# Optimization experiments

Measured on AMD Instinct MI355X. Metric: run time of the kernel, lower is better.

The kernel has to match this reference:

```python
import jax, jax.numpy as jnp
import numpy as np

B, S, H, V, C = 32, 512, 256, 50000, 5
NUM_LAYERS, WINDOW = 2, 2


def setup_inputs() -> dict:
    key = jax.random.key(0)
    ks = jax.random.split(key, 24)
    std = 0.1  # matches nn.init.normal_(p, 0, 0.1)
    n = lambda k, shp: jax.random.normal(k, shp, dtype=jnp.float32) * std
    u = lambda k, shp: -0.05 + jax.random.uniform(k, shp, dtype=jnp.float32) * 0.1
    return {
        "input_sentences": jax.random.randint(ks[0], (B, S), 0, V),
        "sentences_length": jax.random.randint(ks[1], (B,), 1, S),
        "hh0": u(ks[2], (B, S, H)),
        "cs0": u(ks[3], (B, S, H)),
        "embed": n(ks[4], (V, H)),
        # stacked word-gate weights, gate order: i, l, r, f, s, output, u
        "W_lr": n(ks[5], (7, H, 2 * H)),
        "W_c": n(ks[6], (7, H, H)),
        "W_x": n(ks[7], (7, H, H)),
        "W_g": n(ks[8], (7, H, H)),
        "gate_bias": n(ks[9], (7, H)),
        # sentence-state gates
        "W_fg_g": n(ks[10], (H, H)),
        "W_fg_h": n(ks[11], (H, H)),
        "W_fgi_g": n(ks[12], (H, H)),
        "W_fgi_h": n(ks[13], (H, H)),
        "W_og_g": n(ks[14], (H, H)),
        "W_og_h": n(ks[15], (H, H)),
        "b_fg": n(ks[16], (H,)),
        "b_fgi": n(ks[17], (H,)),
        # output head
        "W1": n(ks[18], (H, 2 * H)),
        "b1": n(ks[19], (H,)),
        "Wout": n(ks[20], (C, H)),
        "bout": n(ks[21], (C,)),
    }


def _before_sum(x, window):
    # sum of right-shifted (zero-padded at front) copies, shifts 1..window
    out = jnp.zeros_like(x)
    for s in range(1, window + 1):
        out = out + jnp.pad(x[:, :-s], ((0, 0), (s, 0), (0, 0)))
    return out


def _after_sum(x, window):
    out = jnp.zeros_like(x)
    for s in range(1, window + 1):
        out = out + jnp.pad(x[:, s:], ((0, 0), (0, s), (0, 0)))
    return out


def _slstm_step(hh, cs, sv, scs, wv, W_lr, W_c, W_x, W_g, gate_bias,
                W_fg_g, W_fg_h, W_fgi_g, W_fgi_h, W_og_g, W_og_h, b_fg, b_fgi):
    avg_hh = hh.mean(axis=1)                                   # [B,H]
    f_hat_g = jax.nn.sigmoid(sv @ W_fg_g.T + avg_hh @ W_fg_h.T + b_fg)
    # NOTE: original code (faithfully) uses output_gate_bias here, not output_gate_g_bias
    og_g = jax.nn.sigmoid(sv @ W_og_g.T + avg_hh @ W_og_h.T + gate_bias[5])
    f_hat_g_i = jax.nn.sigmoid((sv @ W_fgi_g.T)[:, None] + hh @ W_fgi_h.T + b_fgi)
    scores = jax.nn.softmax(f_hat_g_i, axis=2)                 # over hidden dim
    new_scs = jax.nn.softmax(f_hat_g, axis=1) * scs + (scores * cs).sum(axis=1)
    new_sv = og_g * jnp.tanh(new_scs)

    hb = _before_sum(hh, WINDOW)
    ha = _after_sum(hh, WINDOW)
    cb = _before_sum(cs, WINDOW)
    ca = _after_sum(cs, WINDOW)
    ba = jnp.concatenate([hb, ha], axis=-1)                    # [B,S,2H]

    # all 7 gate pre-activations at once: [B,S,7,H]
    pre = (jnp.einsum('bsk,ghk->bsgh', ba, W_lr)
           + jnp.einsum('bsk,ghk->bsgh', hh, W_c)
           + jnp.einsum('bsk,ghk->bsgh', wv, W_x)
           + (jnp.einsum('bk,ghk->bgh', new_sv, W_g) + gate_bias)[:, None])

    g5 = jax.nn.sigmoid(pre[..., :5, :])                       # i,l,r,f,s
    b_, s_ = g5.shape[:2]
    # joint softmax over the concatenated 5*H gate vector (as in torch cat+softmax)
    g5 = jax.nn.softmax(g5.reshape(b_, s_, -1), axis=-1).reshape(b_, s_, 5, -1)
    i_t, l_t, r_t, f_t, s_t = (g5[..., k, :] for k in range(5))
    og = jax.nn.sigmoid(pre[..., 5, :])
    u_g = jnp.tanh(pre[..., 6, :])

    new_cs = l_t * cb + f_t * cs + r_t * ca + s_t * scs[:, None] + i_t * u_g
    new_hh = og * jnp.tanh(new_cs)
    return new_hh, new_cs, new_sv, new_scs


def reference(input_sentences, sentences_length, hh0, cs0, embed,
              W_lr, W_c, W_x, W_g, gate_bias,
              W_fg_g, W_fg_h, W_fgi_g, W_fgi_h, W_og_g, W_og_h, b_fg, b_fgi,
              W1, b1, Wout, bout):
    wv = embed[input_sentences]                                # [B,S,H]
    hh, cs = hh0, cs0
    sv, scs = hh0.mean(axis=1), cs0.mean(axis=1)
    for _ in range(NUM_LAYERS):
        hh, cs, sv, scs = _slstm_step(hh, cs, sv, scs, wv,
                                      W_lr, W_c, W_x, W_g, gate_bias,
                                      W_fg_g, W_fg_h, W_fgi_g, W_fgi_h,
                                      W_og_g, W_og_h, b_fg, b_fgi)
    avg_hh = hh.mean(axis=1)
    conc = jnp.concatenate([avg_hh, sv], axis=1) @ W1.T + b1
    fc = conc @ Wout.T + bout
    return jax.nn.log_softmax(fc, axis=1), sv
```

## Files before the change

kernel.cpp:

```cpp
#include <hip/hip_runtime.h>
#include <stdint.h>
#include <math.h>

#define B_   32
#define S_   512
#define H_   256
#define M_   (B_*S_)
#define KBIG 1024
#define NB   1792
#define NB2  2048
#define C_   5

typedef __bf16 bf16;
typedef __bf16 bf16x4 __attribute__((ext_vector_type(4)));
typedef __bf16 bf16x8 __attribute__((ext_vector_type(8)));
typedef float  floatx4 __attribute__((ext_vector_type(4)));

__device__ __forceinline__ float sigm(float x){ return 1.f/(1.f+expf(-x)); }

__device__ __forceinline__ void gl16(const bf16* g, bf16* l){
    __builtin_amdgcn_global_load_lds(
        (const __attribute__((address_space(1))) unsigned int*)g,
        (__attribute__((address_space(3))) unsigned int*)l, 16, 0, 0);
}

__global__ void wcomb_k(const float* __restrict__ Wlr, const float* __restrict__ Wc,
                        const float* __restrict__ Wx, const float* __restrict__ Wfgi,
                        bf16* __restrict__ WT){
    int n = blockIdx.x;
    int k4 = threadIdx.x * 4;
    float4 v;
    if (n < NB){
        int g = n >> 8, h = n & 255;
        const float* src;
        if (k4 < 512)      src = Wlr + ((size_t)(g*256 + h))*512 + k4;
        else if (k4 < 768) src = Wc  + ((size_t)(g*256 + h))*256 + (k4 - 512);
        else               src = Wx  + ((size_t)(g*256 + h))*256 + (k4 - 768);
        v = *(const float4*)src;
    } else {
        int h = n - NB;
        if (k4 >= 512 && k4 < 768) v = *(const float4*)(Wfgi + (size_t)h*H_ + (k4 - 512));
        else { v.x=0.f; v.y=0.f; v.z=0.f; v.w=0.f; }
    }
    bf16 o[4] = {(bf16)v.x,(bf16)v.y,(bf16)v.z,(bf16)v.w};
    *(uint2*)&WT[(size_t)n*KBIG + k4] = *(uint2*)o;
}

__global__ void gather_k(const int* __restrict__ idx, const float* __restrict__ embed,
                         bf16* __restrict__ wv){
    int i4 = (blockIdx.x*256 + threadIdx.x)*4;
    int m = i4 >> 8, h = i4 & 255;
    float4 v = *(const float4*)(embed + (size_t)idx[m]*H_ + h);
    bf16 o[4] = {(bf16)v.x,(bf16)v.y,(bf16)v.z,(bf16)v.w};
    *(uint2*)(wv + (size_t)m*H_ + h) = *(uint2*)o;
}

__global__ void mean1_k(const float* __restrict__ x, float* __restrict__ part){
    int b = blockIdx.x, c = blockIdx.y, h = threadIdx.x;
    const float* p = x + ((size_t)b*S_ + c*32)*H_ + h;
    float s = 0.f;
    #pragma unroll 8
    for (int t=0;t<32;t++) s += p[(size_t)t*H_];
    part[((size_t)b*16 + c)*H_ + h] = s;
}
__global__ void mean2_k(const float* __restrict__ part, float* __restrict__ out){
    int b = blockIdx.x, h = threadIdx.x;
    float s = 0.f;
    #pragma unroll
    for (int c=0;c<16;c++) s += part[((size_t)b*16 + c)*H_ + h];
    out[b*H_ + h] = s * (1.f/512.f);
}

__global__ void buildx_k(const float* __restrict__ hh, const bf16* __restrict__ wv,
                         bf16* __restrict__ X){
    int m = blockIdx.x, tid = threadIdx.x;
    int seg = tid >> 6, li = tid & 63;
    int s = m & (S_-1);
    int h0 = li*4;
    size_t base = (size_t)m*H_ + h0;
    bf16* xr = X + (size_t)m*KBIG + seg*H_ + h0;
    const float4 z = {0.f,0.f,0.f,0.f};
    if (seg == 3){
        *(uint2*)xr = *(const uint2*)&wv[base];
        return;
    }
    float4 v;
    if (seg == 0){
        float4 a = (s>=1) ? *(const float4*)&hh[base - H_]   : z;
        float4 b = (s>=2) ? *(const float4*)&hh[base - 2*H_] : z;
        v.x=a.x+b.x; v.y=a.y+b.y; v.z=a.z+b.z; v.w=a.w+b.w;
    } else if (seg == 1){
        float4 a = (s<=S_-2) ? *(const float4*)&hh[base + H_]   : z;
        float4 b = (s<=S_-3) ? *(const float4*)&hh[base + 2*H_] : z;
        v.x=a.x+b.x; v.y=a.y+b.y; v.z=a.z+b.z; v.w=a.w+b.w;
    } else {
        v = *(const float4*)&hh[base];
    }
    bf16 o[4] = {(bf16)v.x,(bf16)v.y,(bf16)v.z,(bf16)v.w};
    *(uint2*)xr = *(uint2*)o;
}

__global__ void mv5_k(const float* __restrict__ sv, const float* __restrict__ avg,
    const float* __restrict__ Wfg_g, const float* __restrict__ Wfg_h,
    const float* __restrict__ Wog_g, const float* __restrict__ Wog_h,
    const float* __restrict__ Wfgi_g, float* __restrict__ res){
    int j = blockIdx.x, b = blockIdx.y, h = threadIdx.x;
    const float* vec = (j==1 || j==3) ? avg + b*H_ : sv + b*H_;
    const float* W   = (j==0)?Wfg_g:(j==1)?Wfg_h:(j==2)?Wog_g:(j==3)?Wog_h:Wfgi_g;
    __shared__ float v[H_];
    v[h] = vec[h]; __syncthreads();
    const float* w = W + (size_t)h*H_;
    float d = 0.f;
    for (int k=0;k<H_;k++) d += v[k]*w[k];
    res[((size_t)b*5 + j)*H_ + h] = d;
}
__global__ void comb_k(const float* __restrict__ res, const float* __restrict__ b_fg,
                       const float* __restrict__ gbias, const float* __restrict__ b_fgi,
                       float* __restrict__ fhg, float* __restrict__ ogg,
                       float* __restrict__ svg){
    int b = blockIdx.x, h = threadIdx.x;
    const float* r = res + (size_t)b*5*H_;
    fhg[b*H_+h] = sigm(r[h] + r[H_+h] + b_fg[h]);
    ogg[b*H_+h] = sigm(r[2*H_+h] + r[3*H_+h] + gbias[5*H_+h]);
    svg[b*H_+h] = r[4*H_+h] + b_fgi[h];
}

__device__ __forceinline__ void mmq(floatx4 (&acc)[8][4], bf16x8 (&af)[4][2], bf16x8 (&bfr)[2][2],
                                    int MH, int NH){
    #pragma unroll
    for (int mi2=0;mi2<4;mi2++)
        #pragma unroll
        for (int ni2=0;ni2<2;ni2++)
            #pragma unroll
            for (int kk=0;kk<2;kk++)
                acc[MH*4+mi2][NH*2+ni2] = __builtin_amdgcn_mfma_f32_16x16x32_bf16(
                    af[mi2][kk], bfr[ni2][kk], acc[MH*4+mi2][NH*2+ni2], 0, 0, 0);
}

__global__ __launch_bounds__(512, 2)
void mgemm256_k(const bf16* __restrict__ A, const bf16* __restrict__ BT,
                bf16* __restrict__ C, int Kdim, int lda, int ldb, int ldc, int nbx){
    __shared__ alignas(16) bf16 lsA[2][256*64];
    __shared__ alignas(16) bf16 lsB[2][256*64];
    const int tid  = threadIdx.x;
    const int lane = tid & 63;
    const int wave = tid >> 6;
    const int wm = wave >> 2;
    const int wn = wave & 3;
    const int lrow = lane & 15, quad = lane >> 4;

    const int cpx = gridDim.x >> 3;
    const int w   = (blockIdx.x & 7)*cpx + (blockIdx.x >> 3);
    const int mb  = w / nbx, nb = w - mb*nbx;
    const int m0 = mb * 256, n0 = nb * 256;

    const int srow = tid >> 3;
    const int scol = ((tid & 7) ^ (srow & 7)) * 8;
    const bf16* Ab = A  + (size_t)(m0 + srow)*lda + scol;
    const bf16* Bb = BT + (size_t)(n0 + srow)*ldb + scol;
    const int NT = Kdim >> 6;

    floatx4 zero = {0.f,0.f,0.f,0.f};
    floatx4 acc[8][4];
    #pragma unroll
    for (int i=0;i<8;i++)
        #pragma unroll
        for (int j=0;j<4;j++) acc[i][j] = zero;
    bf16x8 af[4][2], bfrA[2][2], bfrB[2][2];

#define SA_(bu,r,kt) gl16(Ab + (size_t)(r)*64*lda + (size_t)(kt)*64, &lsA[bu][(r)*4096 + tid*8])
#define SB_(bu,r,kt) gl16(Bb + (size_t)(r)*64*ldb + (size_t)(kt)*64, &lsB[bu][(r)*4096 + tid*8])
#define RA_(bu,MH,mi2,kk) (*(const bf16x8*)&lsA[bu][(wm*128 + (MH)*64 + (mi2)*16 + lrow)*64 + ((((kk)*4+quad) ^ (lrow&7))*8)])
#define RB_(bu,NH,ni2,kk) (*(const bf16x8*)&lsB[bu][(wn*64  + (NH)*32 + (ni2)*16 + lrow)*64 + ((((kk)*4+quad) ^ (lrow&7))*8)])

    SB_(0,0,0); SB_(0,1,0); SB_(0,2,0); SB_(0,3,0);
    SA_(0,0,0); SA_(0,2,0); SA_(0,1,0); SA_(0,3,0);
    asm volatile("s_waitcnt vmcnt(2)" ::: "memory");
    __builtin_amdgcn_s_barrier();

    for (int kt = 0; kt < NT; ++kt){
        const int cur = kt & 1, nxt = cur ^ 1;
        const bool st = (kt + 1 < NT);
        const int k1 = kt + 1;

        #pragma unroll
        for (int mi2=0;mi2<4;mi2++){ af[mi2][0] = RA_(cur,0,mi2,0); af[mi2][1] = RA_(cur,0,mi2,1); }
        #pragma unroll
        for (int ni2=0;ni2<2;ni2++){ bfrA[ni2][0] = RB_(cur,0,ni2,0); bfrA[ni2][1] = RB_(cur,0,ni2,1); }
        if (st){ SB_(nxt,0,k1); SB_(nxt,1,k1); }
        __builtin_amdgcn_s_barrier();
        __builtin_amdgcn_s_setprio(1);
        mmq(acc, af, bfrA, 0, 0);
        __builtin_amdgcn_s_setprio(0);
        __builtin_amdgcn_s_barrier();

        #pragma unroll
        for (int ni2=0;ni2<2;ni2++){ bfrB[ni2][0] = RB_(cur,1,ni2,0); bfrB[ni2][1] = RB_(cur,1,ni2,1); }
        if (st){ SB_(nxt,2,k1); SB_(nxt,3,k1); }
        __builtin_amdgcn_s_barrier();
        __builtin_amdgcn_s_setprio(1);
        mmq(acc, af, bfrB, 0, 1);
        __builtin_amdgcn_s_setprio(0);
        if (st) asm volatile("s_waitcnt vmcnt(4)" ::: "memory");
        else    asm volatile("s_waitcnt vmcnt(0)" ::: "memory");
        __builtin_amdgcn_s_barrier();

        #pragma unroll
        for (int mi2=0;mi2<4;mi2++){ af[mi2][0] = RA_(cur,1,mi2,0); af[mi2][1] = RA_(cur,1,mi2,1); }
        if (st){ SA_(nxt,0,k1); SA_(nxt,2,k1); }
        __builtin_amdgcn_s_barrier();
        __builtin_amdgcn_s_setprio(1);
        mmq(acc, af, bfrB, 1, 1);
        __builtin_amdgcn_s_setprio(0);
        __builtin_amdgcn_s_barrier();

        if (st){ SA_(nxt,1,k1); SA_(nxt,3,k1); }
        __builtin_amdgcn_s_barrier();
        __builtin_amdgcn_s_setprio(1);
        mmq(acc, af, bfrA, 1, 0);
        __builtin_amdgcn_s_setprio(0);
        if (st) asm volatile("s_waitcnt vmcnt(2)" ::: "memory");
        __builtin_amdgcn_s_barrier();
    }
#undef SA_
#undef SB_
#undef RA_
#undef RB_

    #pragma unroll
    for (int mi=0;mi<8;mi++)
        #pragma unroll
        for (int ni=0;ni<4;ni++){
            int row = m0 + wm*128 + mi*16 + quad*4;
            int col = n0 + wn*64  + ni*16 + lrow;
            #pragma unroll
            for (int r=0;r<4;r++)
                C[(size_t)(row+r)*ldc + col] = (bf16)acc[mi][ni][r];
        }
}

__global__ void scorep_k(const bf16* __restrict__ fgih, const float* __restrict__ svg,
                         const float* __restrict__ cs, float* __restrict__ part, int ldf){
    int chunk = blockIdx.x, b = blockIdx.y;
    int tid = threadIdx.x, wave = tid >> 6, lane = tid & 63;
    __shared__ float acc4[4][256];
    float sw[4], acc[4] = {0.f,0.f,0.f,0.f};
    #pragma unroll
    for (int j=0;j<4;j++) sw[j] = svg[b*H_ + lane + 64*j];
    for (int t=wave; t<16; t+=4){
        int m = b*S_ + chunk*16 + t;
        const bf16* fr = fgih + (size_t)m*ldf;
        float e[4], loc = 0.f;
        #pragma unroll
        for (int j=0;j<4;j++){ e[j] = expf(sigm(sw[j] + (float)fr[lane+64*j])); loc += e[j]; }
        #pragma unroll
        for (int off=32; off; off>>=1) loc += __shfl_xor(loc, off, 64);
        float inv = 1.f/loc;
        const float* cr = cs + (size_t)m*H_;
        #pragma unroll
        for (int j=0;j<4;j++) acc[j] += e[j]*inv*cr[lane+64*j];
    }
    #pragma unroll
    for (int j=0;j<4;j++) acc4[wave][lane+64*j] = acc[j];
    __syncthreads();
    part[((size_t)b*32 + chunk)*H_ + tid] =
        acc4[0][tid] + acc4[1][tid] + acc4[2][tid] + acc4[3][tid];
}

__global__ void newscs_k(const float* __restrict__ part, const float* __restrict__ fhg,
                         const float* __restrict__ ogg, const float* __restrict__ scs_in,
                         float* __restrict__ scs_out, float* __restrict__ sv_out){
    int b = blockIdx.x, h = threadIdx.x;
    __shared__ float r[256];
    float dot = 0.f;
    #pragma unroll 8
    for (int c=0;c<32;c++) dot += part[((size_t)b*32+c)*H_ + h];
    float e = expf(fhg[b*H_+h]);
    r[h] = e; __syncthreads();
    for (int off=128; off; off>>=1){ if (h<off) r[h] += r[h+off]; __syncthreads(); }
    float ns = (e / r[0]) * scs_in[b*H_+h] + dot;
    scs_out[b*H_+h] = ns;
    sv_out[b*H_+h]  = ogg[b*H_+h] * tanhf(ns);
}

__global__ void gterm_k(const float* __restrict__ svn, const float* __restrict__ Wg,
                        const float* __restrict__ gbias, float* __restrict__ gt){
    int g = blockIdx.x, b = blockIdx.y, h = threadIdx.x;
    __shared__ float s[H_];
    s[h] = svn[b*H_+h]; __syncthreads();
    const float* w = Wg + ((size_t)g*H_ + h)*H_;
    float d = 0.f;
    for (int k=0;k<H_;k++) d += s[k]*w[k];
    gt[(size_t)b*NB + g*H_ + h] = d + gbias[g*H_+h];
}

__global__ void gates_k(const bf16* __restrict__ pre, const float* __restrict__ gt,
                        const float* __restrict__ cs_in, const float* __restrict__ scs_in,
                        float* __restrict__ hh_out, float* __restrict__ cs_out, int ldp){
    int tid = threadIdx.x, wave = tid >> 6, lane = tid & 63;
    int m = blockIdx.x*4 + wave;
    int b = m >> 9, s = m & (S_-1);
    const bf16* row = pre + (size_t)m*ldp;
    int h0 = lane*4;
    float pv[7][4];
    #pragma unroll
    for (int g=0; g<7; ++g){
        bf16x4 t = *(const bf16x4*)&row[g*H_ + h0];
        float4 gq = *(const float4*)&gt[(size_t)b*NB + g*H_ + h0];
        pv[g][0] = (float)t[0] + gq.x;
        pv[g][1] = (float)t[1] + gq.y;
        pv[g][2] = (float)t[2] + gq.z;
        pv[g][3] = (float)t[3] + gq.w;
    }
    float ex[5][4], og[4], u[4];
    float loc = 0.f;
    #pragma unroll
    for (int g=0; g<5; ++g)
        #pragma unroll
        for (int j=0;j<4;j++){ float e = expf(sigm(pv[g][j])); ex[g][j] = e; loc += e; }
    #pragma unroll
    for (int j=0;j<4;j++){ og[j] = sigm(pv[5][j]); u[j] = tanhf(pv[6][j]); }
    #pragma unroll
    for (int off=32; off; off>>=1) loc += __shfl_xor(loc, off, 64);
    float inv = 1.f / loc;

    size_t i0 = (size_t)m*H_ + h0;
    const float4 z = {0.f,0.f,0.f,0.f};
    float4 c0  = *(const float4*)&cs_in[i0];
    float4 cm1 = (s>=1)    ? *(const float4*)&cs_in[i0 - H_]   : z;
    float4 cm2 = (s>=2)    ? *(const float4*)&cs_in[i0 - 2*H_] : z;
    float4 cp1 = (s<=S_-2) ? *(const float4*)&cs_in[i0 + H_]   : z;
    float4 cp2 = (s<=S_-3) ? *(const float4*)&cs_in[i0 + 2*H_] : z;
    float4 sc  = *(const float4*)&scs_in[(size_t)b*H_ + h0];
    float4 nc4, nh4;
    #pragma unroll
    for (int j=0;j<4;j++){
        float cb = ((const float*)&cm1)[j] + ((const float*)&cm2)[j];
        float ca = ((const float*)&cp1)[j] + ((const float*)&cp2)[j];
        float nc = ex[1][j]*inv*cb + ex[3][j]*inv*((const float*)&c0)[j] + ex[2][j]*inv*ca
                 + ex[4][j]*inv*((const float*)&sc)[j] + ex[0][j]*inv*u[j];
        ((float*)&nc4)[j] = nc;
        ((float*)&nh4)[j] = og[j] * tanhf(nc);
    }
    *(float4*)&cs_out[i0] = nc4;
    *(float4*)&hh_out[i0] = nh4;
}

__global__ void head_k(const float* __restrict__ avgh, const float* __restrict__ sv,
                       const float* __restrict__ W1, const float* __restrict__ b1,
                       const float* __restrict__ Wout, const float* __restrict__ bout,
                       float* __restrict__ out){
    int b = blockIdx.x, t = threadIdx.x;
    __shared__ float conc[H_];
    __shared__ float fc[8];
    const float* wr = W1 + (size_t)t*512;
    float d = b1[t];
    for (int k=0;k<H_;k++) d += avgh[b*H_+k]*wr[k];
    for (int k=0;k<H_;k++) d += sv[b*H_+k]*wr[256+k];
    conc[t] = d;
    __syncthreads();
    if (t < C_){
        const float* wo = Wout + (size_t)t*H_;
        float s = bout[t];
        for (int i=0;i<H_;i++) s += conc[i]*wo[i];
        fc[t] = s;
    }
    __syncthreads();
    if (t == 0){
        float mx = fc[0];
        for (int c=1;c<C_;c++) mx = fmaxf(mx, fc[c]);
        float se = 0.f;
        for (int c=0;c<C_;c++) se += expf(fc[c]-mx);
        float lse = mx + logf(se);
        for (int c=0;c<C_;c++) out[b*C_+c] = fc[c]-lse;
    }
    out[B_*C_ + b*H_ + t] = sv[b*H_+t];
}

extern "C" void kernel_launch(void* const* d_in, const int* in_sizes, int n_in,
                              void* d_out, int out_size, void* d_ws, size_t ws_size,
                              hipStream_t stream){
    const int*   idx    = (const int*)d_in[0];
    const float* hh0    = (const float*)d_in[2];
    const float* cs0    = (const float*)d_in[3];
    const float* embed  = (const float*)d_in[4];
    const float* Wlr    = (const float*)d_in[5];
    const float* Wc     = (const float*)d_in[6];
    const float* Wx     = (const float*)d_in[7];
    const float* Wg     = (const float*)d_in[8];
    const float* gbias  = (const float*)d_in[9];
    const float* Wfg_g  = (const float*)d_in[10];
    const float* Wfg_h  = (const float*)d_in[11];
    const float* Wfgi_g = (const float*)d_in[12];
    const float* Wfgi_h = (const float*)d_in[13];
    const float* Wog_g  = (const float*)d_in[14];
    const float* Wog_h  = (const float*)d_in[15];
    const float* b_fg   = (const float*)d_in[16];
    const float* b_fgi  = (const float*)d_in[17];
    const float* W1     = (const float*)d_in[18];
    const float* b1     = (const float*)d_in[19];
    const float* Wout   = (const float*)d_in[20];
    const float* bout   = (const float*)d_in[21];

    uint8_t* p = (uint8_t*)d_ws;
    auto alloc = [&](size_t bytes)->void*{ void* r=(void*)p; p += (bytes + 255) & ~(size_t)255; return r; };
    bf16*  WT    = (bf16*)alloc((size_t)NB2*KBIG*2);
    bf16*  X     = (bf16*)alloc((size_t)M_*KBIG*2);
    bf16*  wv    = (bf16*)alloc((size_t)M_*H_*2);
    bf16*  pre   = (bf16*)alloc((size_t)M_*NB2*2);
    float* hhA = (float*)alloc((size_t)M_*H_*4);
    float* csA = (float*)alloc((size_t)M_*H_*4);
    float* hhB = (float*)alloc((size_t)M_*H_*4);
    float* csB = (float*)alloc((size_t)M_*H_*4);
    float* mpart= (float*)alloc((size_t)B_*16*H_*4);
    float* part = (float*)alloc((size_t)B_*32*H_*4);
    float* res5 = (float*)alloc((size_t)B_*5*H_*4);
    float* avgh = (float*)alloc(B_*H_*4);
    float* fhg  = (float*)alloc(B_*H_*4);
    float* ogg  = (float*)alloc(B_*H_*4);
    float* svg  = (float*)alloc(B_*H_*4);
    float* svP0 = (float*)alloc(B_*H_*4);
    float* svP1 = (float*)alloc(B_*H_*4);
    float* scP0 = (float*)alloc(B_*H_*4);
    float* scP1 = (float*)alloc(B_*H_*4);
    float* gt   = (float*)alloc((size_t)B_*NB*4);

    wcomb_k <<<NB2,         256, 0, stream>>>(Wlr, Wc, Wx, Wfgi_h, WT);
    gather_k<<<(M_*H_)/1024,256, 0, stream>>>(idx, embed, wv);
    mean1_k <<<dim3(B_,16), 256, 0, stream>>>(hh0, mpart);
    mean2_k <<<B_,          256, 0, stream>>>(mpart, svP0);
    mean1_k <<<dim3(B_,16), 256, 0, stream>>>(cs0, mpart);
    mean2_k <<<B_,          256, 0, stream>>>(mpart, scP0);

    const float *hin = hh0, *cin = cs0;
    float *hout = hhA, *cout = csA;
    float *svin = svP0, *scin = scP0, *svout = svP1, *scout = scP1;

    for (int l=0; l<2; ++l){
        const float* avgp;
        if (l == 0){
            avgp = svin;
        } else {
            mean1_k<<<dim3(B_,16), 256, 0, stream>>>(hin, mpart);
            mean2_k<<<B_,          256, 0, stream>>>(mpart, avgh);
            avgp = avgh;
        }
        mv5_k   <<<dim3(5,B_), 256, 0, stream>>>(svin, avgp, Wfg_g, Wfg_h, Wog_g,
                                                 Wog_h, Wfgi_g, res5);
        comb_k  <<<B_, 256, 0, stream>>>(res5, b_fg, gbias, b_fgi, fhg, ogg, svg);
        buildx_k<<<M_, 256, 0, stream>>>(hin, wv, X);
        mgemm256_k<<<512, 512, 0, stream>>>(X, WT, pre, KBIG, KBIG, KBIG, NB2, 8);
        scorep_k<<<dim3(32,B_), 256, 0, stream>>>(pre + NB, svg, cin, part, NB2);
        newscs_k<<<B_, 256, 0, stream>>>(part, fhg, ogg, scin, scout, svout);
        gterm_k <<<dim3(7,B_), 256, 0, stream>>>(svout, Wg, gbias, gt);
        gates_k <<<M_/4, 256, 0, stream>>>(pre, gt, cin, scin, hout, cout, NB2);
        hin = hout; cin = cout;
        hout = (l==0) ? hhB : hhA;
        cout = (l==0) ? csB : csA;
        float* q;
        q = svin; svin = svout; svout = q;
        q = scin; scin = scout; scout = q;
    }
    mean1_k<<<dim3(B_,16), 256, 0, stream>>>(hin, mpart);
    mean2_k<<<B_,          256, 0, stream>>>(mpart, avgh);
    head_k <<<B_, 256, 0, stream>>>(avgh, svin, W1, b1, Wout, bout, (float*)d_out);
}
```

Baseline: 516.5 us.

## Simplify GEMM pipeline to one prefetch per tile and fuse gate matvecs

The main GEMM loop drops its interleaved quarter-tile prefetch, which needed many barriers. It now issues all next-tile global-to-LDS loads at the top of each iteration, waits for the previous tile, runs all four MFMA quadrants, and uses a single barrier per k-step. Separately, the five sentence-gate matvecs and their combine step are fused into one kernel per batch row, which removes a launch and the intermediate buffer. The GEMM change cuts synchronisation but may lose the finer overlap of loads with compute. The fused matvec launches only 32 blocks, so it has less parallelism.

```diff
diff --git a/kernel.cpp b/kernel.cpp
--- a/kernel.cpp
+++ b/kernel.cpp
@@ -100,29 +100,31 @@
     *(uint2*)xr = *(uint2*)o;
 }
 
-__global__ void mv5_k(const float* __restrict__ sv, const float* __restrict__ avg,
+__global__ void mv5c_k(const float* __restrict__ sv, const float* __restrict__ avg,
     const float* __restrict__ Wfg_g, const float* __restrict__ Wfg_h,
     const float* __restrict__ Wog_g, const float* __restrict__ Wog_h,
-    const float* __restrict__ Wfgi_g, float* __restrict__ res){
-    int j = blockIdx.x, b = blockIdx.y, h = threadIdx.x;
-    const float* vec = (j==1 || j==3) ? avg + b*H_ : sv + b*H_;
-    const float* W   = (j==0)?Wfg_g:(j==1)?Wfg_h:(j==2)?Wog_g:(j==3)?Wog_h:Wfgi_g;
-    __shared__ float v[H_];
-    v[h] = vec[h]; __syncthreads();
-    const float* w = W + (size_t)h*H_;
-    float d = 0.f;
-    for (int k=0;k<H_;k++) d += v[k]*w[k];
-    res[((size_t)b*5 + j)*H_ + h] = d;
-}
-__global__ void comb_k(const float* __restrict__ res, const float* __restrict__ b_fg,
-                       const float* __restrict__ gbias, const float* __restrict__ b_fgi,
-                       float* __restrict__ fhg, float* __restrict__ ogg,
-                       float* __restrict__ svg){
+    const float* __restrict__ Wfgi_g,
+    const float* __restrict__ b_fg, const float* __restrict__ gbias,
+    const float* __restrict__ b_fgi,
+    float* __restrict__ fhg, float* __restrict__ ogg, float* __restrict__ svg){
     int b = blockIdx.x, h = threadIdx.x;
-    const float* r = res + (size_t)b*5*H_;
-    fhg[b*H_+h] = sigm(r[h] + r[H_+h] + b_fg[h]);
-    ogg[b*H_+h] = sigm(r[2*H_+h] + r[3*H_+h] + gbias[5*H_+h]);
-    svg[b*H_+h] = r[4*H_+h] + b_fgi[h];
+    __shared__ float vs[H_], va[H_];
+    vs[h] = sv[b*H_+h]; va[h] = avg[b*H_+h];
+    __syncthreads();
+    const float* w0 = Wfg_g  + (size_t)h*H_;
+    const float* w1 = Wfg_h  + (size_t)h*H_;
+    const float* w2 = Wog_g  + (size_t)h*H_;
+    const float* w3 = Wog_h  + (size_t)h*H_;
+    const float* w4 = Wfgi_g + (size_t)h*H_;
+    float d0=0.f,d1=0.f,d2=0.f,d3=0.f,d4=0.f;
+    #pragma unroll 4
+    for (int k=0;k<H_;k++){
+        float s = vs[k], a = va[k];
+        d0 += s*w0[k]; d1 += a*w1[k]; d2 += s*w2[k]; d3 += a*w3[k]; d4 += s*w4[k];
+    }
+    fhg[b*H_+h] = sigm(d0 + d1 + b_fg[h]);
+    ogg[b*H_+h] = sigm(d2 + d3 + gbias[5*H_+h]);
+    svg[b*H_+h] = d4 + b_fgi[h];
 }
 
 __device__ __forceinline__ void mmq(floatx4 (&acc)[8][4], bf16x8 (&af)[4][2], bf16x8 (&bfr)[2][2],
@@ -174,8 +176,8 @@
 #define RB_(bu,NH,ni2,kk) (*(const bf16x8*)&lsB[bu][(wn*64  + (NH)*32 + (ni2)*16 + lrow)*64 + ((((kk)*4+quad) ^ (lrow&7))*8)])
 
     SB_(0,0,0); SB_(0,1,0); SB_(0,2,0); SB_(0,3,0);
-    SA_(0,0,0); SA_(0,2,0); SA_(0,1,0); SA_(0,3,0);
-    asm volatile("s_waitcnt vmcnt(2)" ::: "memory");
+    SA_(0,0,0); SA_(0,1,0); SA_(0,2,0); SA_(0,3,0);
+    asm volatile("s_waitcnt vmcnt(0)" ::: "memory");
     __builtin_amdgcn_s_barrier();
 
     for (int kt = 0; kt < NT; ++kt){
@@ -183,43 +185,36 @@
         const bool st = (kt + 1 < NT);
         const int k1 = kt + 1;
 
+        if (st){
+            SB_(nxt,0,k1); SB_(nxt,1,k1); SB_(nxt,2,k1); SB_(nxt,3,k1);
+            SA_(nxt,0,k1); SA_(nxt,1,k1); SA_(nxt,2,k1); SA_(nxt,3,k1);
+            asm volatile("s_waitcnt vmcnt(8)" ::: "memory");
+        } else {
+            asm volatile("s_waitcnt vmcnt(0)" ::: "memory");
+        }
+
         #pragma unroll
         for (int mi2=0;mi2<4;mi2++){ af[mi2][0] = RA_(cur,0,mi2,0); af[mi2][1] = RA_(cur,0,mi2,1); }
         #pragma unroll
         for (int ni2=0;ni2<2;ni2++){ bfrA[ni2][0] = RB_(cur,0,ni2,0); bfrA[ni2][1] = RB_(cur,0,ni2,1); }
-        if (st){ SB_(nxt,0,k1); SB_(nxt,1,k1); }
-        __builtin_amdgcn_s_barrier();
         __builtin_amdgcn_s_setprio(1);
         mmq(acc, af, bfrA, 0, 0);
         __builtin_amdgcn_s_setprio(0);
-        __builtin_amdgcn_s_barrier();
 
         #pragma unroll
         for (int ni2=0;ni2<2;ni2++){ bfrB[ni2][0] = RB_(cur,1,ni2,0); bfrB[ni2][1] = RB_(cur,1,ni2,1); }
-        if (st){ SB_(nxt,2,k1); SB_(nxt,3,k1); }
-        __builtin_amdgcn_s_barrier();
         __builtin_amdgcn_s_setprio(1);
         mmq(acc, af, bfrB, 0, 1);
         __builtin_amdgcn_s_setprio(0);
-        if (st) asm volatile("s_waitcnt vmcnt(4)" ::: "memory");
-        else    asm volatile("s_waitcnt vmcnt(0)" ::: "memory");
-        __builtin_amdgcn_s_barrier();
 
         #pragma unroll
         for (int mi2=0;mi2<4;mi2++){ af[mi2][0] = RA_(cur,1,mi2,0); af[mi2][1] = RA_(cur,1,mi2,1); }
-        if (st){ SA_(nxt,0,k1); SA_(nxt,2,k1); }
-        __builtin_amdgcn_s_barrier();
         __builtin_amdgcn_s_setprio(1);
         mmq(acc, af, bfrB, 1, 1);
-        __builtin_amdgcn_s_setprio(0);
-        __builtin_amdgcn_s_barrier();
-
-        if (st){ SA_(nxt,1,k1); SA_(nxt,3,k1); }
-        __builtin_amdgcn_s_barrier();
-        __builtin_amdgcn_s_setprio(1);
         mmq(acc, af, bfrA, 1, 0);
         __builtin_amdgcn_s_setprio(0);
-        if (st) asm volatile("s_waitcnt vmcnt(2)" ::: "memory");
+
+        asm volatile("s_waitcnt lgkmcnt(0)" ::: "memory");
         __builtin_amdgcn_s_barrier();
     }
 #undef SA_
@@ -414,7 +409,6 @@
     float* csB = (float*)alloc((size_t)M_*H_*4);
     float* mpart= (float*)alloc((size_t)B_*16*H_*4);
     float* part = (float*)alloc((size_t)B_*32*H_*4);
-    float* res5 = (float*)alloc((size_t)B_*5*H_*4);
     float* avgh = (float*)alloc(B_*H_*4);
     float* fhg  = (float*)alloc(B_*H_*4);
     float* ogg  = (float*)alloc(B_*H_*4);
@@ -445,9 +439,8 @@
             mean2_k<<<B_,          256, 0, stream>>>(mpart, avgh);
             avgp = avgh;
         }
-        mv5_k   <<<dim3(5,B_), 256, 0, stream>>>(svin, avgp, Wfg_g, Wfg_h, Wog_g,
-                                                 Wog_h, Wfgi_g, res5);
-        comb_k  <<<B_, 256, 0, stream>>>(res5, b_fg, gbias, b_fgi, fhg, ogg, svg);
+        mv5c_k  <<<B_, 256, 0, stream>>>(svin, avgp, Wfg_g, Wfg_h, Wog_g, Wog_h,
+                                         Wfgi_g, b_fg, gbias, b_fgi, fhg, ogg, svg);
         buildx_k<<<M_, 256, 0, stream>>>(hin, wv, X);
         mgemm256_k<<<512, 512, 0, stream>>>(X, WT, pre, KBIG, KBIG, KBIG, NB2, 8);
         scorep_k<<<dim3(32,B_), 256, 0, stream>>>(pre + NB, svg, cin, part, NB2);
```

Result: slower. 582.2 us (+12.7%).

## Replace 256x256 ping-pong GEMM with simpler 128x128 tile, K=32 kernel

Applied to the files above, without the earlier changes.

Swaps the 256x256-tile, 8-wave GEMM with its interleaved multi-barrier schedule for a 128x128-tile, 4-wave kernel that steps through K 32 at a time with plain double buffering, and launches 2048 blocks instead of 512. The aim is higher occupancy and shorter dependency chains in the per-layer projection GEMM. Each loaded byte is reused less, so global/L2 traffic rises, and there are more barriers per unit of work.

```diff
diff --git a/kernel.cpp b/kernel.cpp
--- a/kernel.cpp
+++ b/kernel.cpp
@@ -125,101 +125,66 @@
     svg[b*H_+h] = r[4*H_+h] + b_fgi[h];
 }
 
-__device__ __forceinline__ void mmq(floatx4 (&acc)[8][4], bf16x8 (&af)[4][2], bf16x8 (&bfr)[2][2],
-                                    int MH, int NH){
-    #pragma unroll
-    for (int mi2=0;mi2<4;mi2++)
-        #pragma unroll
-        for (int ni2=0;ni2<2;ni2++)
-            #pragma unroll
-            for (int kk=0;kk<2;kk++)
-                acc[MH*4+mi2][NH*2+ni2] = __builtin_amdgcn_mfma_f32_16x16x32_bf16(
-                    af[mi2][kk], bfr[ni2][kk], acc[MH*4+mi2][NH*2+ni2], 0, 0, 0);
-}
-
-__global__ __launch_bounds__(512, 2)
-void mgemm256_k(const bf16* __restrict__ A, const bf16* __restrict__ BT,
+__global__ __launch_bounds__(256, 4)
+void mgemm128_k(const bf16* __restrict__ A, const bf16* __restrict__ BT,
                 bf16* __restrict__ C, int Kdim, int lda, int ldb, int ldc, int nbx){
-    __shared__ alignas(16) bf16 lsA[2][256*64];
-    __shared__ alignas(16) bf16 lsB[2][256*64];
+    __shared__ alignas(16) bf16 lsA[2][128*32];
+    __shared__ alignas(16) bf16 lsB[2][128*32];
     const int tid  = threadIdx.x;
     const int lane = tid & 63;
     const int wave = tid >> 6;
-    const int wm = wave >> 2;
-    const int wn = wave & 3;
+    const int wmr = (wave & 1) * 64;
+    const int wnr = (wave >> 1) * 64;
     const int lrow = lane & 15, quad = lane >> 4;
 
     const int cpx = gridDim.x >> 3;
     const int w   = (blockIdx.x & 7)*cpx + (blockIdx.x >> 3);
     const int mb  = w / nbx, nb = w - mb*nbx;
-    const int m0 = mb * 256, n0 = nb * 256;
-
-    const int srow = tid >> 3;
-    const int scol = ((tid & 7) ^ (srow & 7)) * 8;
-    const bf16* Ab = A  + (size_t)(m0 + srow)*lda + scol;
-    const bf16* Bb = BT + (size_t)(n0 + srow)*ldb + scol;
-    const int NT = Kdim >> 6;
+    const int m0 = mb * 128, n0 = nb * 128;
+
+    const int srow  = tid >> 2;
+    const int sslot = (tid & 3) ^ ((srow >> 1) & 3);
+    const bf16* Ab = A  + (size_t)(m0 + srow)*lda + sslot*8;
+    const bf16* Bb = BT + (size_t)(n0 + srow)*ldb + sslot*8;
+    const int NT = Kdim >> 5;
 
     floatx4 zero = {0.f,0.f,0.f,0.f};
-    floatx4 acc[8][4];
-    #pragma unroll
-    for (int i=0;i<8;i++)
+    floatx4 acc[4][4];
+    #pragma unroll
+    for (int i=0;i<4;i++)
         #pragma unroll
         for (int j=0;j<4;j++) acc[i][j] = zero;
-    bf16x8 af[4][2], bfrA[2][2], bfrB[2][2];
-
-#define SA_(bu,r,kt) gl16(Ab + (size_t)(r)*64*lda + (size_t)(kt)*64, &lsA[bu][(r)*4096 + tid*8])
-#define SB_(bu,r,kt) gl16(Bb + (size_t)(r)*64*ldb + (size_t)(kt)*64, &lsB[bu][(r)*4096 + tid*8])
-#define RA_(bu,MH,mi2,kk) (*(const bf16x8*)&lsA[bu][(wm*128 + (MH)*64 + (mi2)*16 + lrow)*64 + ((((kk)*4+quad) ^ (lrow&7))*8)])
-#define RB_(bu,NH,ni2,kk) (*(const bf16x8*)&lsB[bu][(wn*64  + (NH)*32 + (ni2)*16 + lrow)*64 + ((((kk)*4+quad) ^ (lrow&7))*8)])
-
-    SB_(0,0,0); SB_(0,1,0); SB_(0,2,0); SB_(0,3,0);
-    SA_(0,0,0); SA_(0,2,0); SA_(0,1,0); SA_(0,3,0);
-    asm volatile("s_waitcnt vmcnt(2)" ::: "memory");
-    __builtin_amdgcn_s_barrier();
+    bf16x8 af[4], bfr[4];
+
+#define SA_(bu,r,kt) gl16(Ab + (size_t)(r)*64*lda + (size_t)(kt)*32, &lsA[bu][(r)*2048 + tid*8])
+#define SB_(bu,r,kt) gl16(Bb + (size_t)(r)*64*ldb + (size_t)(kt)*32, &lsB[bu][(r)*2048 + tid*8])
+#define RA_(bu,mi) (*(const bf16x8*)&lsA[bu][(wmr + (mi)*16 + lrow)*32 + ((quad ^ ((lrow>>1)&3))*8)])
+#define RB_(bu,ni) (*(const bf16x8*)&lsB[bu][(wnr + (ni)*16 + lrow)*32 + ((quad ^ ((lrow>>1)&3))*8)])
+
+    SA_(0,0,0); SA_(0,1,0); SB_(0,0,0); SB_(0,1,0);
 
     for (int kt = 0; kt < NT; ++kt){
         const int cur = kt & 1, nxt = cur ^ 1;
         const bool st = (kt + 1 < NT);
-        const int k1 = kt + 1;
-
-        #pragma unroll
-        for (int mi2=0;mi2<4;mi2++){ af[mi2][0] = RA_(cur,0,mi2,0); af[mi2][1] = RA_(cur,0,mi2,1); }
-        #pragma unroll
-        for (int ni2=0;ni2<2;ni2++){ bfrA[ni2][0] = RB_(cur,0,ni2,0); bfrA[ni2][1] = RB_(cur,0,ni2,1); }
-        if (st){ SB_(nxt,0,k1); SB_(nxt,1,k1); }
-        __builtin_amdgcn_s_barrier();
-        __builtin_amdgcn_s_setprio(1);
-        mmq(acc, af, bfrA, 0, 0);
-        __builtin_amdgcn_s_setprio(0);
-        __builtin_amdgcn_s_barrier();
-
-        #pragma unroll
-        for (int ni2=0;ni2<2;ni2++){ bfrB[ni2][0] = RB_(cur,1,ni2,0); bfrB[ni2][1] = RB_(cur,1,ni2,1); }
-        if (st){ SB_(nxt,2,k1); SB_(nxt,3,k1); }
-        __builtin_amdgcn_s_barrier();
-        __builtin_amdgcn_s_setprio(1);
-        mmq(acc, af, bfrB, 0, 1);
-        __builtin_amdgcn_s_setprio(0);
+
+        if (st){ SA_(nxt,0,kt+1); SA_(nxt,1,kt+1); SB_(nxt,0,kt+1); SB_(nxt,1,kt+1); }
         if (st) asm volatile("s_waitcnt vmcnt(4)" ::: "memory");
         else    asm volatile("s_waitcnt vmcnt(0)" ::: "memory");
         __builtin_amdgcn_s_barrier();
 
         #pragma unroll
-        for (int mi2=0;mi2<4;mi2++){ af[mi2][0] = RA_(cur,1,mi2,0); af[mi2][1] = RA_(cur,1,mi2,1); }
-        if (st){ SA_(nxt,0,k1); SA_(nxt,2,k1); }
-        __builtin_amdgcn_s_barrier();
+        for (int mi=0;mi<4;mi++) af[mi]  = RA_(cur,mi);
+        #pragma unroll
+        for (int ni=0;ni<4;ni++) bfr[ni] = RB_(cur,ni);
         __builtin_amdgcn_s_setprio(1);
-        mmq(acc, af, bfrB, 1, 1);
+        #pragma unroll
+        for (int mi=0;mi<4;mi++)
+            #pragma unroll
+            for (int ni=0;ni<4;ni++)
+                acc[mi][ni] = __builtin_amdgcn_mfma_f32_16x16x32_bf16(af[mi], bfr[ni], acc[mi][ni], 0, 0, 0);
         __builtin_amdgcn_s_setprio(0);
-        __builtin_amdgcn_s_barrier();
-
-        if (st){ SA_(nxt,1,k1); SA_(nxt,3,k1); }
-        __builtin_amdgcn_s_barrier();
-        __builtin_amdgcn_s_setprio(1);
-        mmq(acc, af, bfrA, 1, 0);
-        __builtin_amdgcn_s_setprio(0);
-        if (st) asm volatile("s_waitcnt vmcnt(2)" ::: "memory");
+
+        asm volatile("s_waitcnt lgkmcnt(0)" ::: "memory");
         __builtin_amdgcn_s_barrier();
     }
 #undef SA_
@@ -228,11 +193,11 @@
 #undef RB_
 
     #pragma unroll
-    for (int mi=0;mi<8;mi++)
+    for (int mi=0;mi<4;mi++)
         #pragma unroll
         for (int ni=0;ni<4;ni++){
-            int row = m0 + wm*128 + mi*16 + quad*4;
-            int col = n0 + wn*64  + ni*16 + lrow;
+            int row = m0 + wmr + mi*16 + quad*4;
+            int col = n0 + wnr + ni*16 + lrow;
             #pragma unroll
             for (int r=0;r<4;r++)
                 C[(size_t)(row+r)*ldc + col] = (bf16)acc[mi][ni][r];
@@ -449,7 +414,7 @@
                                                  Wog_h, Wfgi_g, res5);
         comb_k  <<<B_, 256, 0, stream>>>(res5, b_fg, gbias, b_fgi, fhg, ogg, svg);
         buildx_k<<<M_, 256, 0, stream>>>(hin, wv, X);
-        mgemm256_k<<<512, 512, 0, stream>>>(X, WT, pre, KBIG, KBIG, KBIG, NB2, 8);
+        mgemm128_k<<<2048, 256, 0, stream>>>(X, WT, pre, KBIG, KBIG, KBIG, NB2, 16);
         scorep_k<<<dim3(32,B_), 256, 0, stream>>>(pre + NB, svg, cin, part, NB2);
         newscs_k<<<B_, 256, 0, stream>>>(part, fhg, ogg, scin, scout, svout);
         gterm_k <<<dim3(7,B_), 256, 0, stream>>>(svout, Wg, gbias, gt);
```

New measurement: 526.5 us. No clear change (+1.9%).
